# Kernel tuning notes

Hardware: AMD Instinct MI355X
Metric: run time of the kernel (lower is better)

## Reference

```python
import jax, jax.numpy as jnp
import numpy as np

H = 64          # hidden_dim
N = 100000      # num nodes
E = 1600000     # num edges
L = 3           # num GINEConv layers
VOCAB = 100     # node embedding vocab


def setup_inputs() -> dict:
    key = jax.random.key(0)
    ks = jax.random.split(key, 16)
    s = 0.05
    return {
        "z": jax.random.randint(ks[0], (N,), 0, VOCAB),
        "edge_index": jax.random.randint(ks[1], (2, E), 0, N),
        "edge_attr": jax.random.normal(ks[2], (E, H), dtype=jnp.float32),
        "t": jax.random.uniform(ks[3], (N,), dtype=jnp.float32),
        "emb": jax.random.normal(ks[4], (VOCAB, H), dtype=jnp.float32) * s,
        # reduc_linear: Linear(H+1,H) -> ReLU -> Linear(H,H)
        "rw1": jax.random.normal(ks[5], (H + 1, H), dtype=jnp.float32) * s,
        "rb1": jnp.zeros((H,), dtype=jnp.float32),
        "rw2": jax.random.normal(ks[6], (H, H), dtype=jnp.float32) * s,
        "rb2": jnp.zeros((H,), dtype=jnp.float32),
        # per-conv MLP: Linear(H,H) -> ReLU -> Linear(H,H), stacked over L layers
        "conv_w1": jax.random.normal(ks[7], (L, H, H), dtype=jnp.float32) * s,
        "conv_b1": jnp.zeros((L, H), dtype=jnp.float32),
        "conv_w2": jax.random.normal(ks[8], (L, H, H), dtype=jnp.float32) * s,
        "conv_b2": jnp.zeros((L, H), dtype=jnp.float32),
    }


def _gine_forward(z, edge_index, edge_attr, t, emb, rw1, rb1, rw2, rb2,
                  conv_w1, conv_b1, conv_w2, conv_b2):
    relu = jax.nn.relu
    n = z.shape[0]
    src, dst = edge_index[0], edge_index[1]  # x_j gathered at src, aggregated at dst

    # node embedding + time conditioning
    h = emb[z]                                        # [N, H]
    h = jnp.concatenate([h, t[:, None]], axis=-1)     # [N, H+1]
    h = relu(h @ rw1 + rb1) @ rw2 + rb2               # [N, H]

    for li in range(L):
        # message: relu(x_j + edge_attr); aggregate: scatter-add to dst
        msg = relu(h[src] + edge_attr)                # [E, H]
        agg = jax.ops.segment_sum(msg, dst, num_segments=n)  # [N, H]
        agg = agg + h                                 # (1 + eps) * x_r with eps = 0
        out = relu(agg @ conv_w1[li] + conv_b1[li]) @ conv_w2[li] + conv_b2[li]
        if li < L - 1:
            out = relu(out)
        out = out + h                                 # residual (short_cut)
        h = out
    return h


def reference(z, edge_index, edge_attr, t, emb, rw1, rb1, rw2, rb2,
              conv_w1, conv_b1, conv_w2, conv_b2):
    return _gine_forward(z, edge_index, edge_attr, t, emb, rw1, rb1, rw2, rb2,
                         conv_w1, conv_b1, conv_w2, conv_b2)
```

## Files before the change

kernel.cpp:

```cpp
#include <hip/hip_runtime.h>

#define HD 64

__global__ void __launch_bounds__(256) zero_int_kernel(int* p, long n) {
    long i = blockIdx.x * (long)blockDim.x + threadIdx.x;
    long stride = (long)gridDim.x * blockDim.x;
    for (; i < n; i += stride) p[i] = 0;
}

__global__ void __launch_bounds__(256) hist_kernel(const int* __restrict__ dst,
                                                   int* __restrict__ cnt, long E) {
    long i = blockIdx.x * (long)blockDim.x + threadIdx.x;
    long stride = (long)gridDim.x * blockDim.x;
    for (; i < E; i += stride) atomicAdd(&cnt[dst[i]], 1);
}

__global__ void __launch_bounds__(256) blocksum_kernel(const int* __restrict__ cnt,
                                                       int* __restrict__ bsum, int N) {
    int i = blockIdx.x * 256 + threadIdx.x;
    int v = (i < N) ? cnt[i] : 0;
    #pragma unroll
    for (int off = 32; off; off >>= 1) v += __shfl_down(v, off, 64);
    __shared__ int s[4];
    if ((threadIdx.x & 63) == 0) s[threadIdx.x >> 6] = v;
    __syncthreads();
    if (threadIdx.x == 0) bsum[blockIdx.x] = s[0] + s[1] + s[2] + s[3];
}

__global__ void __launch_bounds__(512) scan2_kernel(const int* __restrict__ bsum,
                                                    int* __restrict__ bpre,
                                                    int* __restrict__ offs,
                                                    int nb, int N, int E) {
    __shared__ int s[512];
    int tid = threadIdx.x;
    int v = (tid < nb) ? bsum[tid] : 0;
    s[tid] = v;
    __syncthreads();
    for (int off = 1; off < 512; off <<= 1) {
        int add = (tid >= off) ? s[tid - off] : 0;
        __syncthreads();
        s[tid] += add;
        __syncthreads();
    }
    if (tid < nb) bpre[tid] = s[tid] - v;
    if (tid == 0) offs[N] = E;
}

__global__ void __launch_bounds__(256) scan3_kernel(const int* __restrict__ cnt,
                                                    const int* __restrict__ bpre,
                                                    int* __restrict__ offs,
                                                    int* __restrict__ cursor, int N) {
    __shared__ int s[256];
    int tid = threadIdx.x;
    int i = blockIdx.x * 256 + tid;
    int v = (i < N) ? cnt[i] : 0;
    s[tid] = v;
    __syncthreads();
    for (int off = 1; off < 256; off <<= 1) {
        int add = (tid >= off) ? s[tid - off] : 0;
        __syncthreads();
        s[tid] += add;
        __syncthreads();
    }
    if (i < N) {
        int excl = s[tid] - v + bpre[blockIdx.x];
        offs[i] = excl;
        cursor[i] = excl;
    }
}

__global__ void __launch_bounds__(256) fill_kernel(const int* __restrict__ src,
                                                   const int* __restrict__ dst,
                                                   int* __restrict__ cursor,
                                                   int* __restrict__ perm,
                                                   int* __restrict__ sp, long E) {
    long i = blockIdx.x * (long)blockDim.x + threadIdx.x;
    long stride = (long)gridDim.x * blockDim.x;
    for (; i < E; i += stride) {
        int d = dst[i];
        int p = atomicAdd(&cursor[d], 1);
        perm[p] = (int)i;
        sp[p]   = src[i];
    }
}

__global__ void __launch_bounds__(512, 6) node_init_kernel(
    const int* __restrict__ z, const float* __restrict__ t,
    const float* __restrict__ emb,
    const float* __restrict__ rw1, const float* __restrict__ rb1,
    const float* __restrict__ rw2, const float* __restrict__ rb2,
    float* __restrict__ h, int N)
{
    __shared__ float s_w1[65 * 64];
    __shared__ float s_w2[64 * 64];
    __shared__ float s_x[8][66];
    __shared__ float s_y1[8][64];

    int tid = threadIdx.x;
    for (int i = tid; i < 65 * 64; i += 512) s_w1[i] = rw1[i];
    for (int i = tid; i < 64 * 64; i += 512) s_w2[i] = rw2[i];
    __syncthreads();

    int wv = tid >> 6;
    int c  = tid & 63;
    float b1 = rb1[c];
    float b2 = rb2[c];

    long stride = (long)gridDim.x * 8;
    for (long base = (long)blockIdx.x * 8; base < N; base += stride) {
        long node = base + wv;
        if (node >= N) continue;
        s_x[wv][c] = emb[(long)z[node] * HD + c];
        if (c == 0) s_x[wv][64] = t[node];
        float acc = b1;
        #pragma unroll
        for (int k = 0; k < 65; ++k)
            acc = fmaf(s_x[wv][k], s_w1[k * 64 + c], acc);
        s_y1[wv][c] = fmaxf(acc, 0.f);
        float acc2 = b2;
        #pragma unroll
        for (int k = 0; k < 64; ++k)
            acc2 = fmaf(s_y1[wv][k], s_w2[k * 64 + c], acc2);
        h[node * HD + c] = acc2;
    }
}

__global__ void __launch_bounds__(512, 6) layer_kernel(
    const int* __restrict__ offs, const int* __restrict__ perm,
    const int* __restrict__ sp,
    const float* __restrict__ h, const float* __restrict__ ea,
    const float* __restrict__ w1, const float* __restrict__ b1,
    const float* __restrict__ w2, const float* __restrict__ b2,
    float* __restrict__ out, int N, int relu_flag)
{
    __shared__ float s_w1[64 * 64];
    __shared__ float s_w2[64 * 64];
    __shared__ float s_x[8][64];
    __shared__ float s_y1[8][64];

    int tid = threadIdx.x;
    for (int i = tid; i < 64 * 64; i += 512) {
        s_w1[i] = w1[i];
        s_w2[i] = w2[i];
    }
    __syncthreads();

    int wv   = tid >> 6;
    int lane = tid & 63;
    int c    = lane;
    int eg   = lane >> 4;
    int cq   = (lane & 15) * 4;
    float bb1 = b1[c];
    float bb2 = b2[c];

    long stride = (long)gridDim.x * 8;
    for (long base = (long)blockIdx.x * 8; base < N; base += stride) {
        long node = base + wv;
        if (node >= N) continue;

        int jb = offs[node], je = offs[node + 1];
        float hval = h[node * HD + c];

        float4 acc; acc.x = acc.y = acc.z = acc.w = 0.f;
        int j = jb + eg;
        int e = 0, s = 0;
        if (j < je) { e = perm[j]; s = sp[j]; }
        while (j < je) {
            const float4 av = *(const float4*)(ea + (long)e * HD + cq);
            const float4 hv = *(const float4*)(h  + (long)s * HD + cq);
            int jn = j + 4;
            int en = 0, sn = 0;
            if (jn < je) { en = perm[jn]; sn = sp[jn]; }
            acc.x += fmaxf(av.x + hv.x, 0.f);
            acc.y += fmaxf(av.y + hv.y, 0.f);
            acc.z += fmaxf(av.z + hv.z, 0.f);
            acc.w += fmaxf(av.w + hv.w, 0.f);
            j = jn; e = en; s = sn;
        }
        #pragma unroll
        for (int m = 16; m <= 32; m <<= 1) {
            acc.x += __shfl_xor(acc.x, m, 64);
            acc.y += __shfl_xor(acc.y, m, 64);
            acc.z += __shfl_xor(acc.z, m, 64);
            acc.w += __shfl_xor(acc.w, m, 64);
        }
        if (lane < 16) *(float4*)&s_x[wv][cq] = acc;
        s_x[wv][c] += hval;

        float a1 = bb1;
        #pragma unroll
        for (int k = 0; k < 64; ++k)
            a1 = fmaf(s_x[wv][k], s_w1[k * 64 + c], a1);
        s_y1[wv][c] = fmaxf(a1, 0.f);

        float a2 = bb2;
        #pragma unroll
        for (int k = 0; k < 64; ++k)
            a2 = fmaf(s_y1[wv][k], s_w2[k * 64 + c], a2);
        if (relu_flag) a2 = fmaxf(a2, 0.f);
        out[node * HD + c] = a2 + hval;
    }
}

extern "C" void kernel_launch(void* const* d_in, const int* in_sizes, int n_in,
                              void* d_out, int out_size, void* d_ws, size_t ws_size,
                              hipStream_t stream)
{
    const int*   z    = (const int*)  d_in[0];
    const int*   ei   = (const int*)  d_in[1];
    const float* ea   = (const float*)d_in[2];
    const float* t    = (const float*)d_in[3];
    const float* emb  = (const float*)d_in[4];
    const float* rw1  = (const float*)d_in[5];
    const float* rb1  = (const float*)d_in[6];
    const float* rw2  = (const float*)d_in[7];
    const float* rb2  = (const float*)d_in[8];
    const float* cw1  = (const float*)d_in[9];
    const float* cb1  = (const float*)d_in[10];
    const float* cw2  = (const float*)d_in[11];
    const float* cb2  = (const float*)d_in[12];

    int  N = in_sizes[0];
    long E = (long)in_sizes[1] / 2;
    const int* src = ei;
    const int* dst = ei + E;

    float* out = (float*)d_out;

    float* bufA   = (float*)d_ws;
    int*   offs   = (int*)(bufA + (long)N * HD);
    int*   cursor = offs + (N + 1);
    int*   perm   = cursor + N;
    int*   sp     = perm + E;
    int*   bsum   = sp + E;
    int    nb     = (N + 255) / 256;
    int*   bpre   = bsum + nb;

    zero_int_kernel<<<256, 256, 0, stream>>>(cursor, N);
    hist_kernel<<<2048, 256, 0, stream>>>(dst, cursor, E);
    blocksum_kernel<<<nb, 256, 0, stream>>>(cursor, bsum, N);
    scan2_kernel<<<1, 512, 0, stream>>>(bsum, bpre, offs, nb, N, (int)E);
    scan3_kernel<<<nb, 256, 0, stream>>>(cursor, bpre, offs, cursor, N);
    fill_kernel<<<2048, 256, 0, stream>>>(src, dst, cursor, perm, sp, E);

    node_init_kernel<<<1024, 512, 0, stream>>>(z, t, emb, rw1, rb1, rw2, rb2,
                                               bufA, N);

    float* hcur = bufA;
    for (int li = 0; li < 3; ++li) {
        float* hout = (li == 1) ? bufA : out;
        layer_kernel<<<1024, 512, 0, stream>>>(
            offs, perm, sp, hcur, ea,
            cw1 + (long)li * HD * HD, cb1 + (long)li * HD,
            cw2 + (long)li * HD * HD, cb2 + (long)li * HD,
            hout, N, (li < 2) ? 1 : 0);
        hcur = hout;
    }
}
```

Measured before the change: 1.129 ms.

## Process two nodes per wavefront to interleave edge gathers and share weight reads

```diff
diff --git a/kernel.cpp b/kernel.cpp
--- a/kernel.cpp
+++ b/kernel.cpp
@@ -93,35 +93,52 @@
 {
     __shared__ float s_w1[65 * 64];
     __shared__ float s_w2[64 * 64];
-    __shared__ float s_x[8][66];
-    __shared__ float s_y1[8][64];
+    __shared__ float s_x[16][66];
 
     int tid = threadIdx.x;
     for (int i = tid; i < 65 * 64; i += 512) s_w1[i] = rw1[i];
     for (int i = tid; i < 64 * 64; i += 512) s_w2[i] = rw2[i];
     __syncthreads();
 
-    int wv = tid >> 6;
-    int c  = tid & 63;
+    int wv  = tid >> 6;
+    int c   = tid & 63;
+    int wv2 = wv << 1;
     float b1 = rb1[c];
     float b2 = rb2[c];
 
-    long stride = (long)gridDim.x * 8;
-    for (long base = (long)blockIdx.x * 8; base < N; base += stride) {
-        long node = base + wv;
-        if (node >= N) continue;
-        s_x[wv][c] = emb[(long)z[node] * HD + c];
-        if (c == 0) s_x[wv][64] = t[node];
-        float acc = b1;
-        #pragma unroll
-        for (int k = 0; k < 65; ++k)
-            acc = fmaf(s_x[wv][k], s_w1[k * 64 + c], acc);
-        s_y1[wv][c] = fmaxf(acc, 0.f);
-        float acc2 = b2;
-        #pragma unroll
-        for (int k = 0; k < 64; ++k)
-            acc2 = fmaf(s_y1[wv][k], s_w2[k * 64 + c], acc2);
-        h[node * HD + c] = acc2;
+    long stride = (long)gridDim.x * 16;
+    for (long base = (long)blockIdx.x * 16; base < N; base += stride) {
+        long node0 = base + (long)wv2;
+        if (node0 >= N) continue;
+        long node1 = node0 + 1;
+        bool v1 = (node1 < N);
+
+        s_x[wv2][c] = emb[(long)z[node0] * HD + c];
+        if (c == 0) s_x[wv2][64] = t[node0];
+        if (v1) {
+            s_x[wv2 + 1][c] = emb[(long)z[node1] * HD + c];
+            if (c == 0) s_x[wv2 + 1][64] = t[node1];
+        }
+
+        float a10 = b1, a11 = b1;
+        #pragma unroll
+        for (int k = 0; k < 65; ++k) {
+            float w = s_w1[k * 64 + c];
+            a10 = fmaf(s_x[wv2][k],     w, a10);
+            a11 = fmaf(s_x[wv2 + 1][k], w, a11);
+        }
+        s_x[wv2][c]     = fmaxf(a10, 0.f);
+        s_x[wv2 + 1][c] = fmaxf(a11, 0.f);
+
+        float a20 = b2, a21 = b2;
+        #pragma unroll
+        for (int k = 0; k < 64; ++k) {
+            float w = s_w2[k * 64 + c];
+            a20 = fmaf(s_x[wv2][k],     w, a20);
+            a21 = fmaf(s_x[wv2 + 1][k], w, a21);
+        }
+        h[node0 * HD + c] = a20;
+        if (v1) h[node1 * HD + c] = a21;
     }
 }
 
@@ -135,8 +152,7 @@
 {
     __shared__ float s_w1[64 * 64];
     __shared__ float s_w2[64 * 64];
-    __shared__ float s_x[8][64];
-    __shared__ float s_y1[8][64];
+    __shared__ float s_x[16][64];
 
     int tid = threadIdx.x;
     for (int i = tid; i < 64 * 64; i += 512) {
@@ -150,55 +166,95 @@
     int c    = lane;
     int eg   = lane >> 4;
     int cq   = (lane & 15) * 4;
+    int wv2  = wv << 1;
     float bb1 = b1[c];
     float bb2 = b2[c];
 
-    long stride = (long)gridDim.x * 8;
-    for (long base = (long)blockIdx.x * 8; base < N; base += stride) {
-        long node = base + wv;
-        if (node >= N) continue;
-
-        int jb = offs[node], je = offs[node + 1];
-        float hval = h[node * HD + c];
-
-        float4 acc; acc.x = acc.y = acc.z = acc.w = 0.f;
-        int j = jb + eg;
-        int e = 0, s = 0;
-        if (j < je) { e = perm[j]; s = sp[j]; }
-        while (j < je) {
-            const float4 av = *(const float4*)(ea + (long)e * HD + cq);
-            const float4 hv = *(const float4*)(h  + (long)s * HD + cq);
-            int jn = j + 4;
-            int en = 0, sn = 0;
-            if (jn < je) { en = perm[jn]; sn = sp[jn]; }
-            acc.x += fmaxf(av.x + hv.x, 0.f);
-            acc.y += fmaxf(av.y + hv.y, 0.f);
-            acc.z += fmaxf(av.z + hv.z, 0.f);
-            acc.w += fmaxf(av.w + hv.w, 0.f);
-            j = jn; e = en; s = sn;
+    long stride = (long)gridDim.x * 16;
+    for (long base = (long)blockIdx.x * 16; base < N; base += stride) {
+        long node0 = base + (long)wv2;
+        if (node0 >= N) continue;
+        long node1 = node0 + 1;
+        bool v1 = (node1 < N);
+
+        int jb0 = offs[node0], je0 = offs[node0 + 1];
+        int jb1 = 0, je1 = 0;
+        float hval0 = h[node0 * HD + c];
+        float hval1 = 0.f;
+        if (v1) {
+            jb1 = offs[node1]; je1 = offs[node1 + 1];
+            hval1 = h[node1 * HD + c];
+        }
+
+        float4 acc0; acc0.x = acc0.y = acc0.z = acc0.w = 0.f;
+        float4 acc1 = acc0;
+        int j0 = jb0 + eg, j1 = jb1 + eg;
+        int e0 = 0, s0 = 0, e1 = 0, s1 = 0;
+        if (j0 < je0) { e0 = perm[j0]; s0 = sp[j0]; }
+        if (j1 < je1) { e1 = perm[j1]; s1 = sp[j1]; }
+        while (j0 < je0 || j1 < je1) {
+            bool p0 = j0 < je0, p1 = j1 < je1;
+            const float4 av0 = *(const float4*)(ea + (long)e0 * HD + cq);
+            const float4 hv0 = *(const float4*)(h  + (long)s0 * HD + cq);
+            const float4 av1 = *(const float4*)(ea + (long)e1 * HD + cq);
+            const float4 hv1 = *(const float4*)(h  + (long)s1 * HD + cq);
+            int jn0 = j0 + 4, jn1 = j1 + 4;
+            int en0 = e0, sn0 = s0, en1 = e1, sn1 = s1;
+            if (jn0 < je0) { en0 = perm[jn0]; sn0 = sp[jn0]; }
+            if (jn1 < je1) { en1 = perm[jn1]; sn1 = sp[jn1]; }
+            if (p0) {
+                acc0.x += fmaxf(av0.x + hv0.x, 0.f);
+                acc0.y += fmaxf(av0.y + hv0.y, 0.f);
+                acc0.z += fmaxf(av0.z + hv0.z, 0.f);
+                acc0.w += fmaxf(av0.w + hv0.w, 0.f);
+            }
+            if (p1) {
+                acc1.x += fmaxf(av1.x + hv1.x, 0.f);
+                acc1.y += fmaxf(av1.y + hv1.y, 0.f);
+                acc1.z += fmaxf(av1.z + hv1.z, 0.f);
+                acc1.w += fmaxf(av1.w + hv1.w, 0.f);
+            }
+            j0 = jn0; j1 = jn1;
+            e0 = en0; s0 = sn0; e1 = en1; s1 = sn1;
         }
         #pragma unroll
         for (int m = 16; m <= 32; m <<= 1) {
-            acc.x += __shfl_xor(acc.x, m, 64);
-            acc.y += __shfl_xor(acc.y, m, 64);
-            acc.z += __shfl_xor(acc.z, m, 64);
-            acc.w += __shfl_xor(acc.w, m, 64);
-        }
-        if (lane < 16) *(float4*)&s_x[wv][cq] = acc;
-        s_x[wv][c] += hval;
-
-        float a1 = bb1;
-        #pragma unroll
-        for (int k = 0; k < 64; ++k)
-            a1 = fmaf(s_x[wv][k], s_w1[k * 64 + c], a1);
-        s_y1[wv][c] = fmaxf(a1, 0.f);
-
-        float a2 = bb2;
-        #pragma unroll
-        for (int k = 0; k < 64; ++k)
-            a2 = fmaf(s_y1[wv][k], s_w2[k * 64 + c], a2);
-        if (relu_flag) a2 = fmaxf(a2, 0.f);
-        out[node * HD + c] = a2 + hval;
+            acc0.x += __shfl_xor(acc0.x, m, 64);
+            acc0.y += __shfl_xor(acc0.y, m, 64);
+            acc0.z += __shfl_xor(acc0.z, m, 64);
+            acc0.w += __shfl_xor(acc0.w, m, 64);
+            acc1.x += __shfl_xor(acc1.x, m, 64);
+            acc1.y += __shfl_xor(acc1.y, m, 64);
+            acc1.z += __shfl_xor(acc1.z, m, 64);
+            acc1.w += __shfl_xor(acc1.w, m, 64);
+        }
+        if (lane < 32) {
+            float4 a = (lane < 16) ? acc0 : acc1;
+            *(float4*)&s_x[wv2 + (lane >> 4)][cq] = a;
+        }
+        s_x[wv2][c]     += hval0;
+        s_x[wv2 + 1][c] += hval1;
+
+        float a10 = bb1, a11 = bb1;
+        #pragma unroll
+        for (int k = 0; k < 64; ++k) {
+            float w = s_w1[k * 64 + c];
+            a10 = fmaf(s_x[wv2][k],     w, a10);
+            a11 = fmaf(s_x[wv2 + 1][k], w, a11);
+        }
+        s_x[wv2][c]     = fmaxf(a10, 0.f);
+        s_x[wv2 + 1][c] = fmaxf(a11, 0.f);
+
+        float a20 = bb2, a21 = bb2;
+        #pragma unroll
+        for (int k = 0; k < 64; ++k) {
+            float w = s_w2[k * 64 + c];
+            a20 = fmaf(s_x[wv2][k],     w, a20);
+            a21 = fmaf(s_x[wv2 + 1][k], w, a21);
+        }
+        if (relu_flag) { a20 = fmaxf(a20, 0.f); a21 = fmaxf(a21, 0.f); }
+        out[node0 * HD + c] = a20 + hval0;
+        if (v1) out[node1 * HD + c] = a21 + hval1;
     }
 }
 
```

Measured after the change: 1.342 ms. 18.8% more time.

## Split layer into 4-deep unrolled gather kernel and register-blocked MLP kernel

Applied to the files above, without the earlier changes.

```diff
diff --git a/kernel.cpp b/kernel.cpp
--- a/kernel.cpp
+++ b/kernel.cpp
@@ -72,15 +72,13 @@
 __global__ void __launch_bounds__(256) fill_kernel(const int* __restrict__ src,
                                                    const int* __restrict__ dst,
                                                    int* __restrict__ cursor,
-                                                   int* __restrict__ perm,
-                                                   int* __restrict__ sp, long E) {
+                                                   int2* __restrict__ ps, long E) {
     long i = blockIdx.x * (long)blockDim.x + threadIdx.x;
     long stride = (long)gridDim.x * blockDim.x;
     for (; i < E; i += stride) {
         int d = dst[i];
         int p = atomicAdd(&cursor[d], 1);
-        perm[p] = (int)i;
-        sp[p]   = src[i];
+        ps[p] = make_int2((int)i, src[i]);
     }
 }
 
@@ -125,80 +123,142 @@
     }
 }
 
-__global__ void __launch_bounds__(512, 6) layer_kernel(
-    const int* __restrict__ offs, const int* __restrict__ perm,
-    const int* __restrict__ sp,
+__global__ void __launch_bounds__(256, 8) gather_kernel(
+    const int* __restrict__ offs, const int2* __restrict__ ps,
     const float* __restrict__ h, const float* __restrict__ ea,
+    float* __restrict__ agg, int N)
+{
+    int tid  = threadIdx.x;
+    int wv   = tid >> 6;
+    int lane = tid & 63;
+    int eg   = lane >> 4;
+    int cq   = (lane & 15) * 4;
+
+    long nw = (long)gridDim.x * 4;
+    for (long node = (long)blockIdx.x * 4 + wv; node < N; node += nw) {
+        int jb = offs[node], je = offs[node + 1];
+        float4 acc; acc.x = acc.y = acc.z = acc.w = 0.f;
+
+        for (int j0 = jb + eg; j0 < je; j0 += 16) {
+            int2  pp[4];
+            float m[4];
+            #pragma unroll
+            for (int u = 0; u < 4; ++u) {
+                int jj = j0 + u * 4;
+                bool v = jj < je;
+                m[u]  = v ? 1.f : 0.f;
+                pp[u] = ps[v ? jj : jb];
+            }
+            float4 av[4], hv[4];
+            #pragma unroll
+            for (int u = 0; u < 4; ++u) {
+                av[u] = *(const float4*)(ea + (long)pp[u].x * HD + cq);
+                hv[u] = *(const float4*)(h  + (long)pp[u].y * HD + cq);
+            }
+            #pragma unroll
+            for (int u = 0; u < 4; ++u) {
+                acc.x = fmaf(m[u], fmaxf(av[u].x + hv[u].x, 0.f), acc.x);
+                acc.y = fmaf(m[u], fmaxf(av[u].y + hv[u].y, 0.f), acc.y);
+                acc.z = fmaf(m[u], fmaxf(av[u].z + hv[u].z, 0.f), acc.z);
+                acc.w = fmaf(m[u], fmaxf(av[u].w + hv[u].w, 0.f), acc.w);
+            }
+        }
+        #pragma unroll
+        for (int mm = 16; mm <= 32; mm <<= 1) {
+            acc.x += __shfl_xor(acc.x, mm, 64);
+            acc.y += __shfl_xor(acc.y, mm, 64);
+            acc.z += __shfl_xor(acc.z, mm, 64);
+            acc.w += __shfl_xor(acc.w, mm, 64);
+        }
+        if (lane < 16) {
+            const float4 hh = *(const float4*)(h + node * HD + cq);
+            acc.x += hh.x; acc.y += hh.y; acc.z += hh.z; acc.w += hh.w;
+            *(float4*)(agg + node * HD + cq) = acc;
+        }
+    }
+}
+
+__global__ void __launch_bounds__(512, 6) mlp_kernel(
+    const float* __restrict__ x, const float* __restrict__ hres,
     const float* __restrict__ w1, const float* __restrict__ b1,
     const float* __restrict__ w2, const float* __restrict__ b2,
     float* __restrict__ out, int N, int relu_flag)
 {
     __shared__ float s_w1[64 * 64];
     __shared__ float s_w2[64 * 64];
-    __shared__ float s_x[8][64];
-    __shared__ float s_y1[8][64];
+    __shared__ float s_x[8][512];
 
     int tid = threadIdx.x;
     for (int i = tid; i < 64 * 64; i += 512) {
-        s_w1[i] = w1[i];
-        s_w2[i] = w2[i];
-    }
-    __syncthreads();
-
-    int wv   = tid >> 6;
-    int lane = tid & 63;
-    int c    = lane;
-    int eg   = lane >> 4;
-    int cq   = (lane & 15) * 4;
+        int k = i >> 6, cc = i & 63;
+        int q = k >> 2, r = k & 3;
+        int idx = (cc << 6) + ((q ^ (cc & 7)) << 2) + r;
+        s_w1[idx] = w1[i];
+        s_w2[idx] = w2[i];
+    }
+    __syncthreads();
+
+    int wv = tid >> 6;
+    int c  = tid & 63;
+    float* sx = s_x[wv];
+    int wbase = c << 6;
+    int wsel  = (c & 7) << 2;
     float bb1 = b1[c];
     float bb2 = b2[c];
 
-    long stride = (long)gridDim.x * 8;
-    for (long base = (long)blockIdx.x * 8; base < N; base += stride) {
-        long node = base + wv;
-        if (node >= N) continue;
-
-        int jb = offs[node], je = offs[node + 1];
-        float hval = h[node * HD + c];
-
-        float4 acc; acc.x = acc.y = acc.z = acc.w = 0.f;
-        int j = jb + eg;
-        int e = 0, s = 0;
-        if (j < je) { e = perm[j]; s = sp[j]; }
-        while (j < je) {
-            const float4 av = *(const float4*)(ea + (long)e * HD + cq);
-            const float4 hv = *(const float4*)(h  + (long)s * HD + cq);
-            int jn = j + 4;
-            int en = 0, sn = 0;
-            if (jn < je) { en = perm[jn]; sn = sp[jn]; }
-            acc.x += fmaxf(av.x + hv.x, 0.f);
-            acc.y += fmaxf(av.y + hv.y, 0.f);
-            acc.z += fmaxf(av.z + hv.z, 0.f);
-            acc.w += fmaxf(av.w + hv.w, 0.f);
-            j = jn; e = en; s = sn;
-        }
-        #pragma unroll
-        for (int m = 16; m <= 32; m <<= 1) {
-            acc.x += __shfl_xor(acc.x, m, 64);
-            acc.y += __shfl_xor(acc.y, m, 64);
-            acc.z += __shfl_xor(acc.z, m, 64);
-            acc.w += __shfl_xor(acc.w, m, 64);
-        }
-        if (lane < 16) *(float4*)&s_x[wv][cq] = acc;
-        s_x[wv][c] += hval;
-
-        float a1 = bb1;
-        #pragma unroll
-        for (int k = 0; k < 64; ++k)
-            a1 = fmaf(s_x[wv][k], s_w1[k * 64 + c], a1);
-        s_y1[wv][c] = fmaxf(a1, 0.f);
-
-        float a2 = bb2;
-        #pragma unroll
-        for (int k = 0; k < 64; ++k)
-            a2 = fmaf(s_y1[wv][k], s_w2[k * 64 + c], a2);
-        if (relu_flag) a2 = fmaxf(a2, 0.f);
-        out[node * HD + c] = a2 + hval;
+    long ngroups = (long)(N + 7) >> 3;
+    long gstride = (long)gridDim.x * 8;
+    for (long g = (long)blockIdx.x * 8 + wv; g < ngroups; g += gstride) {
+        long base = g << 3;
+
+        {
+            const float4 v0 = *(const float4*)(x + base * HD + (c << 3));
+            const float4 v1 = *(const float4*)(x + base * HD + (c << 3) + 4);
+            *(float4*)&sx[(c << 3)]     = v0;
+            *(float4*)&sx[(c << 3) + 4] = v1;
+        }
+        float hr[8];
+        #pragma unroll
+        for (int n = 0; n < 8; ++n) hr[n] = hres[(base + n) * HD + c];
+
+        float acc[8];
+        #pragma unroll
+        for (int n = 0; n < 8; ++n) acc[n] = bb1;
+        #pragma unroll
+        for (int q = 0; q < 16; ++q) {
+            const float4 wq = *(const float4*)&s_w1[wbase + ((q << 2) ^ wsel)];
+            #pragma unroll
+            for (int n = 0; n < 8; ++n) {
+                const float4 xq = *(const float4*)&sx[(n << 6) + (q << 2)];
+                acc[n] = fmaf(xq.x, wq.x, acc[n]);
+                acc[n] = fmaf(xq.y, wq.y, acc[n]);
+                acc[n] = fmaf(xq.z, wq.z, acc[n]);
+                acc[n] = fmaf(xq.w, wq.w, acc[n]);
+            }
+        }
+        #pragma unroll
+        for (int n = 0; n < 8; ++n) sx[(n << 6) + c] = fmaxf(acc[n], 0.f);
+
+        #pragma unroll
+        for (int n = 0; n < 8; ++n) acc[n] = bb2;
+        #pragma unroll
+        for (int q = 0; q < 16; ++q) {
+            const float4 wq = *(const float4*)&s_w2[wbase + ((q << 2) ^ wsel)];
+            #pragma unroll
+            for (int n = 0; n < 8; ++n) {
+                const float4 xq = *(const float4*)&sx[(n << 6) + (q << 2)];
+                acc[n] = fmaf(xq.x, wq.x, acc[n]);
+                acc[n] = fmaf(xq.y, wq.y, acc[n]);
+                acc[n] = fmaf(xq.z, wq.z, acc[n]);
+                acc[n] = fmaf(xq.w, wq.w, acc[n]);
+            }
+        }
+        #pragma unroll
+        for (int n = 0; n < 8; ++n) {
+            float v = acc[n];
+            if (relu_flag) v = fmaxf(v, 0.f);
+            out[(base + n) * HD + c] = v + hr[n];
+        }
     }
 }
 
@@ -230,9 +290,8 @@
     float* bufA   = (float*)d_ws;
     int*   offs   = (int*)(bufA + (long)N * HD);
     int*   cursor = offs + (N + 1);
-    int*   perm   = cursor + N;
-    int*   sp     = perm + E;
-    int*   bsum   = sp + E;
+    int2*  ps     = (int2*)(cursor + N + 1);
+    int*   bsum   = (int*)(ps + E);
     int    nb     = (N + 255) / 256;
     int*   bpre   = bsum + nb;
 
@@ -241,7 +300,7 @@
     blocksum_kernel<<<nb, 256, 0, stream>>>(cursor, bsum, N);
     scan2_kernel<<<1, 512, 0, stream>>>(bsum, bpre, offs, nb, N, (int)E);
     scan3_kernel<<<nb, 256, 0, stream>>>(cursor, bpre, offs, cursor, N);
-    fill_kernel<<<2048, 256, 0, stream>>>(src, dst, cursor, perm, sp, E);
+    fill_kernel<<<2048, 256, 0, stream>>>(src, dst, cursor, ps, E);
 
     node_init_kernel<<<1024, 512, 0, stream>>>(z, t, emb, rw1, rb1, rw2, rb2,
                                                bufA, N);
@@ -249,8 +308,9 @@
     float* hcur = bufA;
     for (int li = 0; li < 3; ++li) {
         float* hout = (li == 1) ? bufA : out;
-        layer_kernel<<<1024, 512, 0, stream>>>(
-            offs, perm, sp, hcur, ea,
+        gather_kernel<<<8192, 256, 0, stream>>>(offs, ps, hcur, ea, hout, N);
+        mlp_kernel<<<1568, 512, 0, stream>>>(
+            hout, hcur,
             cw1 + (long)li * HD * HD, cb1 + (long)li * HD,
             cw2 + (long)li * HD * HD, cb2 + (long)li * HD,
             hout, N, (li < 2) ? 1 : 0);
```

After: 1.272 ms. 1.13x slower.

## Fuse three GINE layer launches into one persistent kernel with grid barrier

Applied to the files above, without the earlier changes.

```diff
diff --git a/kernel.cpp b/kernel.cpp
--- a/kernel.cpp
+++ b/kernel.cpp
@@ -125,80 +125,107 @@
     }
 }
 
-__global__ void __launch_bounds__(512, 6) layer_kernel(
+__device__ __forceinline__ void grid_sync(int* cnt, int* gen, int nblocks) {
+    __syncthreads();
+    if (threadIdx.x == 0) {
+        __threadfence();
+        int g = atomicAdd(gen, 0);
+        if (atomicAdd(cnt, 1) == nblocks - 1) {
+            atomicExch(cnt, 0);
+            __threadfence();
+            atomicAdd(gen, 1);
+        } else {
+            while (atomicAdd(gen, 0) == g) __builtin_amdgcn_s_sleep(1);
+        }
+        __threadfence();
+    }
+    __syncthreads();
+}
+
+__global__ void __launch_bounds__(512, 6) layers_persistent_kernel(
     const int* __restrict__ offs, const int* __restrict__ perm,
-    const int* __restrict__ sp,
-    const float* __restrict__ h, const float* __restrict__ ea,
-    const float* __restrict__ w1, const float* __restrict__ b1,
-    const float* __restrict__ w2, const float* __restrict__ b2,
-    float* __restrict__ out, int N, int relu_flag)
+    const int* __restrict__ sp, const float* __restrict__ ea,
+    float* __restrict__ bufA, float* __restrict__ dout,
+    const float* __restrict__ cw1, const float* __restrict__ cb1,
+    const float* __restrict__ cw2, const float* __restrict__ cb2,
+    int* __restrict__ bar, int N, int nblocks)
 {
     __shared__ float s_w1[64 * 64];
     __shared__ float s_w2[64 * 64];
     __shared__ float s_x[8][64];
     __shared__ float s_y1[8][64];
 
-    int tid = threadIdx.x;
-    for (int i = tid; i < 64 * 64; i += 512) {
-        s_w1[i] = w1[i];
-        s_w2[i] = w2[i];
-    }
-    __syncthreads();
-
+    int tid  = threadIdx.x;
     int wv   = tid >> 6;
     int lane = tid & 63;
     int c    = lane;
     int eg   = lane >> 4;
     int cq   = (lane & 15) * 4;
-    float bb1 = b1[c];
-    float bb2 = b2[c];
-
-    long stride = (long)gridDim.x * 8;
-    for (long base = (long)blockIdx.x * 8; base < N; base += stride) {
-        long node = base + wv;
-        if (node >= N) continue;
-
-        int jb = offs[node], je = offs[node + 1];
-        float hval = h[node * HD + c];
-
-        float4 acc; acc.x = acc.y = acc.z = acc.w = 0.f;
-        int j = jb + eg;
-        int e = 0, s = 0;
-        if (j < je) { e = perm[j]; s = sp[j]; }
-        while (j < je) {
-            const float4 av = *(const float4*)(ea + (long)e * HD + cq);
-            const float4 hv = *(const float4*)(h  + (long)s * HD + cq);
-            int jn = j + 4;
-            int en = 0, sn = 0;
-            if (jn < je) { en = perm[jn]; sn = sp[jn]; }
-            acc.x += fmaxf(av.x + hv.x, 0.f);
-            acc.y += fmaxf(av.y + hv.y, 0.f);
-            acc.z += fmaxf(av.z + hv.z, 0.f);
-            acc.w += fmaxf(av.w + hv.w, 0.f);
-            j = jn; e = en; s = sn;
+
+    for (int li = 0; li < 3; ++li) {
+        const float* w1 = cw1 + (long)li * HD * HD;
+        const float* w2 = cw2 + (long)li * HD * HD;
+        for (int i = tid; i < 64 * 64; i += 512) {
+            s_w1[i] = w1[i];
+            s_w2[i] = w2[i];
         }
-        #pragma unroll
-        for (int m = 16; m <= 32; m <<= 1) {
-            acc.x += __shfl_xor(acc.x, m, 64);
-            acc.y += __shfl_xor(acc.y, m, 64);
-            acc.z += __shfl_xor(acc.z, m, 64);
-            acc.w += __shfl_xor(acc.w, m, 64);
+        __syncthreads();
+
+        const float* h   = (li == 1) ? dout : bufA;
+        float*       out = (li == 1) ? bufA : dout;
+        int relu_flag = (li < 2) ? 1 : 0;
+        float bb1 = cb1[li * HD + c];
+        float bb2 = cb2[li * HD + c];
+
+        long stride = (long)gridDim.x * 8;
+        for (long base = (long)blockIdx.x * 8; base < N; base += stride) {
+            long node = base + wv;
+            if (node >= N) continue;
+
+            int jb = offs[node], je = offs[node + 1];
+            float hval = h[node * HD + c];
+
+            float4 acc; acc.x = acc.y = acc.z = acc.w = 0.f;
+            int j = jb + eg;
+            int e = 0, s = 0;
+            if (j < je) { e = perm[j]; s = sp[j]; }
+            while (j < je) {
+                const float4 av = *(const float4*)(ea + (long)e * HD + cq);
+                const float4 hv = *(const float4*)(h  + (long)s * HD + cq);
+                int jn = j + 4;
+                int en = 0, sn = 0;
+                if (jn < je) { en = perm[jn]; sn = sp[jn]; }
+                acc.x += fmaxf(av.x + hv.x, 0.f);
+                acc.y += fmaxf(av.y + hv.y, 0.f);
+                acc.z += fmaxf(av.z + hv.z, 0.f);
+                acc.w += fmaxf(av.w + hv.w, 0.f);
+                j = jn; e = en; s = sn;
+            }
+            #pragma unroll
+            for (int m = 16; m <= 32; m <<= 1) {
+                acc.x += __shfl_xor(acc.x, m, 64);
+                acc.y += __shfl_xor(acc.y, m, 64);
+                acc.z += __shfl_xor(acc.z, m, 64);
+                acc.w += __shfl_xor(acc.w, m, 64);
+            }
+            if (lane < 16) *(float4*)&s_x[wv][cq] = acc;
+            s_x[wv][c] += hval;
+
+            float a1 = bb1;
+            #pragma unroll
+            for (int k = 0; k < 64; ++k)
+                a1 = fmaf(s_x[wv][k], s_w1[k * 64 + c], a1);
+            s_y1[wv][c] = fmaxf(a1, 0.f);
+
+            float a2 = bb2;
+            #pragma unroll
+            for (int k = 0; k < 64; ++k)
+                a2 = fmaf(s_y1[wv][k], s_w2[k * 64 + c], a2);
+            if (relu_flag) a2 = fmaxf(a2, 0.f);
+            out[node * HD + c] = a2 + hval;
         }
-        if (lane < 16) *(float4*)&s_x[wv][cq] = acc;
-        s_x[wv][c] += hval;
-
-        float a1 = bb1;
-        #pragma unroll
-        for (int k = 0; k < 64; ++k)
-            a1 = fmaf(s_x[wv][k], s_w1[k * 64 + c], a1);
-        s_y1[wv][c] = fmaxf(a1, 0.f);
-
-        float a2 = bb2;
-        #pragma unroll
-        for (int k = 0; k < 64; ++k)
-            a2 = fmaf(s_y1[wv][k], s_w2[k * 64 + c], a2);
-        if (relu_flag) a2 = fmaxf(a2, 0.f);
-        out[node * HD + c] = a2 + hval;
+
+        if (li < 2) grid_sync(bar, bar + 1, nblocks);
     }
 }
 
@@ -235,8 +262,10 @@
     int*   bsum   = sp + E;
     int    nb     = (N + 255) / 256;
     int*   bpre   = bsum + nb;
+    int*   bar    = bpre + nb;
 
     zero_int_kernel<<<256, 256, 0, stream>>>(cursor, N);
+    zero_int_kernel<<<1, 256, 0, stream>>>(bar, 2);
     hist_kernel<<<2048, 256, 0, stream>>>(dst, cursor, E);
     blocksum_kernel<<<nb, 256, 0, stream>>>(cursor, bsum, N);
     scan2_kernel<<<1, 512, 0, stream>>>(bsum, bpre, offs, nb, N, (int)E);
@@ -246,14 +275,7 @@
     node_init_kernel<<<1024, 512, 0, stream>>>(z, t, emb, rw1, rb1, rw2, rb2,
                                                bufA, N);
 
-    float* hcur = bufA;
-    for (int li = 0; li < 3; ++li) {
-        float* hout = (li == 1) ? bufA : out;
-        layer_kernel<<<1024, 512, 0, stream>>>(
-            offs, perm, sp, hcur, ea,
-            cw1 + (long)li * HD * HD, cb1 + (long)li * HD,
-            cw2 + (long)li * HD * HD, cb2 + (long)li * HD,
-            hout, N, (li < 2) ? 1 : 0);
-        hcur = hout;
-    }
-}
+    layers_persistent_kernel<<<768, 512, 0, stream>>>(
+        offs, perm, sp, ea, bufA, out,
+        cw1, cb1, cw2, cb2, bar, N, 768);
+}
```

After: 1.319 ms. +16.8%, slower.
